# Kernel tuning notes

Measured on AMD Instinct MI355X. Metric: run time of the kernel, lower is better.

Reference implementation:

```python
import jax, jax.numpy as jnp
import numpy as np

B, C, IMG, P = 32, 3, 224, 16
D, DEPTH, N, K, E = 384, 12, 16, 4, 2
DI = E * D           # 768
R = (D + 15) // 16   # dt_rank = 24
L = (IMG // P) ** 2  # 196
NC = 1000


def _layernorm(x, g, b, eps=1e-5):
    mu = jnp.mean(x, axis=-1, keepdims=True)
    var = jnp.var(x, axis=-1, keepdims=True)
    return (x - mu) * jax.lax.rsqrt(var + eps) * g + b


def _block(x, p):
    bn_g, bn_b, in_w, conv_w, conv_b, xp_w, dtp_w, dtp_b, A_log, Dsk, out_w = p
    h = _layernorm(x, bn_g, bn_b)
    xz = h @ in_w                       # (B,L,2*DI)
    xc, z = xz[..., :DI], xz[..., DI:]
    # causal depthwise conv1d along L
    xpad = jnp.pad(xc, ((0, 0), (K - 1, 0), (0, 0)))
    xc = sum(conv_w[:, k] * xpad[:, k:k + L, :] for k in range(K)) + conv_b
    xc = jax.nn.silu(xc)
    dbc = xc @ xp_w                      # (B,L,R+2N)
    dt, Bm, Cm = dbc[..., :R], dbc[..., R:R + N], dbc[..., R + N:]
    dt = jax.nn.softplus(dt @ dtp_w + dtp_b)        # (B,L,DI)
    A = -jnp.exp(A_log)                              # (DI,N)
    da = jnp.exp(dt[..., None] * A)                  # (B,L,DI,N)
    db = dt[..., None] * Bm[:, :, None, :] * xc[..., None]
    def combine(c1, c2):
        a1, b1 = c1
        a2, b2 = c2
        return a1 * a2, a2 * b1 + b2
    _, hs = jax.lax.associative_scan(combine, (da, db), axis=1)
    y = jnp.einsum('blmn,bln->blm', hs, Cm) + Dsk * xc
    y = y * jax.nn.silu(z)
    return x + y @ out_w


def setup_inputs() -> dict:
    key = jax.random.key(0)
    ks = jax.random.split(key, 16)
    s = 0.02
    inp = {
        'x': jax.random.normal(ks[0], (B, C, IMG, IMG), jnp.float32),
        'patch_w': jax.random.normal(ks[1], (D, C, P, P), jnp.float32) * s,
        'patch_b': jnp.zeros((D,), jnp.float32),
        'pos_embed': jax.random.normal(ks[2], (1, L, D), jnp.float32) * s,
        'bn_g': jnp.ones((DEPTH, D), jnp.float32),
        'bn_b': jnp.zeros((DEPTH, D), jnp.float32),
        'in_w': jax.random.normal(ks[3], (DEPTH, D, 2 * DI), jnp.float32) * s,
        'conv_w': jax.random.normal(ks[4], (DEPTH, DI, K), jnp.float32) * s,
        'conv_b': jnp.zeros((DEPTH, DI), jnp.float32),
        'xp_w': jax.random.normal(ks[5], (DEPTH, DI, R + 2 * N), jnp.float32) * s,
        'dtp_w': jax.random.normal(ks[6], (DEPTH, R, DI), jnp.float32) * (R ** -0.5),
        'dtp_b': jax.random.uniform(ks[7], (DEPTH, DI), jnp.float32, -4.0, -1.0),
        'A_log': jnp.log(jnp.broadcast_to(jnp.arange(1, N + 1, dtype=jnp.float32), (DEPTH, DI, N))),
        'D_skip': jnp.ones((DEPTH, DI), jnp.float32),
        'out_w': jax.random.normal(ks[8], (DEPTH, DI, D), jnp.float32) * s,
        'norm_g': jnp.ones((D,), jnp.float32),
        'norm_b': jnp.zeros((D,), jnp.float32),
        'head_w': jax.random.normal(ks[9], (D, NC), jnp.float32) * s,
        'head_b': jnp.zeros((NC,), jnp.float32),
    }
    return inp


def reference(x, patch_w, patch_b, pos_embed, bn_g, bn_b, in_w, conv_w, conv_b,
              xp_w, dtp_w, dtp_b, A_log, D_skip, out_w, norm_g, norm_b, head_w, head_b):
    # patch embed: conv2d stride=patch -> (B,D,H',W') -> (B,L,D) + pos
    h = jax.lax.conv_general_dilated(x, patch_w, (P, P), 'VALID',
                                     dimension_numbers=('NCHW', 'OIHW', 'NCHW'))
    h = h + patch_b[None, :, None, None]
    h = h.reshape(B, D, L).transpose(0, 2, 1) + pos_embed
    params = (bn_g, bn_b, in_w, conv_w, conv_b, xp_w, dtp_w, dtp_b, A_log, D_skip, out_w)
    h, _ = jax.lax.scan(lambda c, p: (_block(c, p), None), h, params)
    h = _layernorm(h, norm_g, norm_b)
    feat = h.mean(axis=1)
    return feat @ head_w + head_b
```

## Files before the change

### kernel.cpp

```cpp
#include <hip/hip_runtime.h>
#include <math.h>

typedef short bf16x8 __attribute__((ext_vector_type(8)));
typedef float f32x4 __attribute__((ext_vector_type(4)));
typedef float f32x2 __attribute__((ext_vector_type(2)));
typedef unsigned short u16;
typedef unsigned int u32;
typedef unsigned short u16x4 __attribute__((ext_vector_type(4)));

#define B_    32
#define D_    384
#define DEPTH 12
#define NST   16
#define DI_   768
#define R_    24
#define L_    196
#define NC_   1000
#define M_    (B_*L_)
#define SEG   28
#define NSEG  7

__device__ __forceinline__ u16 f2bf(float f) {
  union { float f; unsigned u; } v; v.f = f;
  unsigned r = v.u + 0x7fffu + ((v.u >> 16) & 1u);
  return (u16)(r >> 16);
}
__device__ __forceinline__ float bf2f(u16 x) {
  union { unsigned u; float f; } v; v.u = ((unsigned)x) << 16;
  return v.f;
}
__device__ __forceinline__ float quad_sum(float y) {
  y += __int_as_float(__builtin_amdgcn_update_dpp(0, __float_as_int(y), 0xB1, 0xf, 0xf, true));
  y += __int_as_float(__builtin_amdgcn_update_dpp(0, __float_as_int(y), 0x4E, 0xf, 0xf, true));
  return y;
}

__global__ void k_transpose_bf16(const float* __restrict__ in, u16* __restrict__ out,
                                 int R, int C) {
  __shared__ float tile[32][33];
  const size_t zoff = (size_t)blockIdx.z * R * C;
  in  += zoff; out += zoff;
  int c0 = blockIdx.x * 32, r0 = blockIdx.y * 32;
  int tx = threadIdx.x, ty = threadIdx.y;
  for (int i = ty; i < 32; i += 8) {
    int r = r0 + i, c = c0 + tx;
    tile[i][tx] = (r < R && c < C) ? in[(size_t)r * C + c] : 0.f;
  }
  __syncthreads();
  for (int i = ty; i < 32; i += 8) {
    int c = c0 + i, r = r0 + tx;
    if (c < C && r < R) out[(size_t)c * R + r] = f2bf(tile[tx][i]);
  }
}

__global__ void k_convert_bf16(const float* __restrict__ in, u16* __restrict__ out, int n) {
  int i = blockIdx.x * 256 + threadIdx.x;
  if (i < n) out[i] = f2bf(in[i]);
}

__global__ void k_prepA(const float* __restrict__ alog, float* __restrict__ A, int n) {
  int i = blockIdx.x * 256 + threadIdx.x;
  if (i < n) A[i] = -__expf(alog[i]);
}

__global__ void k_im2col(const float* __restrict__ x, u16* __restrict__ xcol) {
  int idx = blockIdx.x * 256 + threadIdx.x;
  if (idx >= M_ * 768) return;
  int k = idx % 768, m = idx / 768;
  int b = m / L_, l = m % L_;
  int li = l / 14, lj = l % 14;
  int c = k / 256, r = k % 256;
  int i = r / 16, j = r % 16;
  int hh = li * 16 + i, ww = lj * 16 + j;
  xcol[idx] = f2bf(x[(((size_t)b * 3 + c) * 224 + hh) * 224 + ww]);
}

template<int BM, int BN, int EPI, int OB>
__global__ __launch_bounds__(256)
void k_gemm(const u16* __restrict__ A, const u16* __restrict__ BT,
            float* __restrict__ Cout, int Nn, int Kk,
            const float* __restrict__ bias, const float* __restrict__ pos) {
  const int m0 = blockIdx.x * BM;
  const int n0 = blockIdx.y * BN;
  __shared__ u16 lA[BM * 72];
  __shared__ u16 lB[BN * 72];
  const int tid  = threadIdx.x;
  const int wave = tid >> 6, lane = tid & 63;
  const int wm = (wave >> 1) * (BM / 2), wn = (wave & 1) * (BN / 2);
  constexpr int MI = BM / 32, NJ = BN / 32;
  constexpr int NV = (BM + BN) / 32;
  f32x4 acc[MI][NJ] = {};
  const int fr = lane & 15, kg = (lane >> 4) * 8;

  bf16x8 v[NV];
  auto load = [&](int k0) {
    #pragma unroll
    for (int q = 0; q < NV; ++q) {
      int id = tid + q * 256;
      int row = id >> 3, vv = id & 7;
      bf16x8 t = {};
      if (row < BM) {
        t = *(const bf16x8*)(A + (size_t)(m0 + row) * Kk + k0 + vv * 8);
      } else {
        int br = n0 + row - BM;
        if (br < Nn) t = *(const bf16x8*)(BT + (size_t)br * Kk + k0 + vv * 8);
      }
      v[q] = t;
    }
  };
  load(0);
  for (int k0 = 0; k0 < Kk; k0 += 64) {
    __syncthreads();
    #pragma unroll
    for (int q = 0; q < NV; ++q) {
      int id = tid + q * 256;
      int row = id >> 3, vv = id & 7;
      u16* dst = (row < BM) ? (lA + row * 72 + vv * 8) : (lB + (size_t)(row - BM) * 72 + vv * 8);
      *(bf16x8*)dst = v[q];
    }
    __syncthreads();
    if (k0 + 64 < Kk) load(k0 + 64);
    #pragma unroll
    for (int kk = 0; kk < 64; kk += 32) {
      bf16x8 af[MI], bfr[NJ];
      #pragma unroll
      for (int i = 0; i < MI; ++i)
        af[i] = *(const bf16x8*)(lA + (wm + i * 16 + fr) * 72 + kk + kg);
      #pragma unroll
      for (int j = 0; j < NJ; ++j)
        bfr[j] = *(const bf16x8*)(lB + (wn + j * 16 + fr) * 72 + kk + kg);
      #pragma unroll
      for (int i = 0; i < MI; ++i)
        #pragma unroll
        for (int j = 0; j < NJ; ++j)
          acc[i][j] = __builtin_amdgcn_mfma_f32_16x16x32_bf16(af[i], bfr[j], acc[i][j], 0, 0, 0);
    }
  }

  const int rg = (lane >> 4) * 4;
  #pragma unroll
  for (int i = 0; i < MI; ++i) {
    int row = m0 + wm + i * 16 + rg;
    #pragma unroll
    for (int j = 0; j < NJ; ++j) {
      int col = n0 + wn + j * 16 + fr;
      if (col >= Nn) continue;
      #pragma unroll
      for (int r = 0; r < 4; ++r) {
        float vv = acc[i][j][r];
        size_t idx = (size_t)(row + r) * Nn + col;
        if (EPI == 0) {
          if (OB) ((u16*)Cout)[idx] = f2bf(vv);
          else    Cout[idx] = vv;
        }
        else if (EPI == 1) Cout[idx] += vv;
        else               Cout[idx] = vv + bias[col] + pos[(size_t)((row + r) % L_) * Nn + col];
      }
    }
  }
}

__global__ __launch_bounds__(256)
void k_xp_split(const u16* __restrict__ A, const u16* __restrict__ BT,
                float* __restrict__ pbuf) {
  const int m0 = blockIdx.x * 32;
  const int ks = blockIdx.y;
  __shared__ u16 lA[32 * 72];
  __shared__ u16 lB[64 * 72];
  const int tid  = threadIdx.x;
  const int wave = tid >> 6, lane = tid & 63;
  const int wm = (wave >> 1) * 16, wn = (wave & 1) * 32;
  const int fr = lane & 15, kg = (lane >> 4) * 8;
  f32x4 acc[2] = {};

  bf16x8 v[3];
  auto load = [&](int k0) {
    #pragma unroll
    for (int q = 0; q < 3; ++q) {
      int id = tid + q * 256;
      int row = id >> 3, vv = id & 7;
      bf16x8 t = {};
      if (row < 32) {
        t = *(const bf16x8*)(A + (size_t)(m0 + row) * DI_ + k0 + vv * 8);
      } else {
        int br = row - 32;
        if (br < 56) t = *(const bf16x8*)(BT + (size_t)br * DI_ + k0 + vv * 8);
      }
      v[q] = t;
    }
  };
  const int kbase = ks * 192;
  load(kbase);
  for (int k0 = kbase; k0 < kbase + 192; k0 += 64) {
    __syncthreads();
    #pragma unroll
    for (int q = 0; q < 3; ++q) {
      int id = tid + q * 256;
      int row = id >> 3, vv = id & 7;
      u16* dst = (row < 32) ? (lA + row * 72 + vv * 8) : (lB + (size_t)(row - 32) * 72 + vv * 8);
      *(bf16x8*)dst = v[q];
    }
    __syncthreads();
    if (k0 + 64 < kbase + 192) load(k0 + 64);
    #pragma unroll
    for (int kk = 0; kk < 64; kk += 32) {
      bf16x8 af = *(const bf16x8*)(lA + (wm + fr) * 72 + kk + kg);
      bf16x8 b0 = *(const bf16x8*)(lB + (wn + fr) * 72 + kk + kg);
      bf16x8 b1 = *(const bf16x8*)(lB + (wn + 16 + fr) * 72 + kk + kg);
      acc[0] = __builtin_amdgcn_mfma_f32_16x16x32_bf16(af, b0, acc[0], 0, 0, 0);
      acc[1] = __builtin_amdgcn_mfma_f32_16x16x32_bf16(af, b1, acc[1], 0, 0, 0);
    }
  }
  const int rg = (lane >> 4) * 4;
  #pragma unroll
  for (int j = 0; j < 2; ++j) {
    int col = wn + j * 16 + fr;
    if (col >= 56) continue;
    #pragma unroll
    for (int r = 0; r < 4; ++r) {
      int row = wm + rg + r;
      pbuf[((size_t)ks * M_ + m0 + row) * 56 + col] = acc[j][r];
    }
  }
}

__global__ __launch_bounds__(384)
void k_ln(const float* __restrict__ x, const float* __restrict__ g,
          const float* __restrict__ bt, u16* __restrict__ h) {
  const int m = blockIdx.x, d = threadIdx.x;
  __shared__ float red[12];
  float v = x[(size_t)m * D_ + d];
  float s = v, s2 = v * v;
  #pragma unroll
  for (int o = 32; o > 0; o >>= 1) { s += __shfl_xor(s, o); s2 += __shfl_xor(s2, o); }
  int wid = d >> 6;
  if ((d & 63) == 0) { red[wid] = s; red[6 + wid] = s2; }
  __syncthreads();
  float ts = 0.f, ts2 = 0.f;
  #pragma unroll
  for (int w = 0; w < 6; ++w) { ts += red[w]; ts2 += red[6 + w]; }
  float mu = ts / (float)D_;
  float var = ts2 / (float)D_ - mu * mu;
  float rs = rsqrtf(var + 1e-5f);
  h[(size_t)m * D_ + d] = f2bf((v - mu) * rs * g[d] + bt[d]);
}

__global__ __launch_bounds__(256)
void k_conv(const u16* __restrict__ xzb, const float* __restrict__ cw,
            const float* __restrict__ cb, u16* __restrict__ xcb) {
  int idx = blockIdx.x * 256 + threadIdx.x;
  if (idx >= M_ * (DI_ / 4)) return;
  int dq = idx % (DI_ / 4), m = idx / (DI_ / 4), l = m % L_;
  int di4 = dq * 4;
  const u16* base = xzb + (size_t)m * 1536 + di4;
  float xv[4][4];
  #pragma unroll
  for (int t = 0; t < 4; ++t) {
    int back = 3 - t;
    u16x4 v = {};
    if (l >= back) v = *(const u16x4*)(base - (size_t)back * 1536);
    #pragma unroll
    for (int c = 0; c < 4; ++c) xv[t][c] = bf2f(v[c]);
  }
  f32x4 bv = *(const f32x4*)(cb + di4);
  u16x4 outv;
  #pragma unroll
  for (int c = 0; c < 4; ++c) {
    f32x4 w = *(const f32x4*)(cw + (size_t)(di4 + c) * 4);
    float acc = bv[c] + w[0] * xv[0][c] + w[1] * xv[1][c] + w[2] * xv[2][c] + w[3] * xv[3][c];
    float s = acc / (1.f + __expf(-acc));
    outv[c] = f2bf(s);
  }
  *(u16x4*)(xcb + (size_t)m * DI_ + di4) = outv;
}

__global__ __launch_bounds__(256)
void k_scan_part(const float* __restrict__ pbuf, const u16* __restrict__ xcb,
                 const float* __restrict__ dtw, const float* __restrict__ dtb,
                 const float* __restrict__ Abuf, const float* __restrict__ Dsk,
                 float* __restrict__ ys, float* __restrict__ hend,
                 float* __restrict__ send) {
  const int b   = blockIdx.x;
  const int di0 = blockIdx.y * 64;
  const int s   = blockIdx.z;
  const int tid = threadIdx.x;
  const int dil = tid >> 2, nq = tid & 3;
  const int di  = di0 + dil;
  __shared__ float sDT[SEG][64];
  __shared__ float sXC[SEG][64];
  __shared__ float sBC[SEG][32];
  __shared__ float sdb[SEG][28];

  const f32x4 Arow = *(const f32x4*)(Abuf + (size_t)di * NST + nq * 4);
  const float Dv = Dsk[di];
  const size_t mb = (size_t)b * L_ + (size_t)s * SEG;
  const int chd = tid & 63;

  {
    int r = tid >> 4, cc = (tid & 15) * 4;
    #pragma unroll
    for (int j = 0; j < 2; ++j) {
      int row = r + j * 16;
      if (row < SEG) {
        u16x4 xv = *(const u16x4*)(xcb + (mb + row) * DI_ + di0 + cc);
        f32x4 xf;
        #pragma unroll
        for (int q = 0; q < 4; ++q) xf[q] = bf2f(xv[q]);
        *(f32x4*)&sXC[row][cc] = xf;
      }
    }
    if (tid < SEG * 6) {
      int row = tid / 6, c4 = (tid % 6) * 4;
      f32x4 ssum = {};
      #pragma unroll
      for (int ks = 0; ks < 4; ++ks)
        ssum += *(const f32x4*)(pbuf + ((size_t)ks * M_ + mb + row) * 56 + c4);
      *(f32x4*)&sdb[row][c4] = ssum;
    }
    if (tid < SEG * 8) {
      int row = tid >> 3, c4 = (tid & 7) * 4;
      f32x4 ssum = {};
      #pragma unroll
      for (int ks = 0; ks < 4; ++ks)
        ssum += *(const f32x4*)(pbuf + ((size_t)ks * M_ + mb + row) * 56 + 24 + c4);
      *(f32x4*)&sBC[row][c4] = ssum;
    }
  }
  float w[24];
  #pragma unroll
  for (int r = 0; r < 24; ++r) w[r] = dtw[r * DI_ + di0 + chd];
  const float bvd = dtb[di0 + chd];
  __syncthreads();

  {
    const int rg = tid >> 6;
    #pragma unroll
    for (int rr = 0; rr < 7; ++rr) {
      int row = rg * 7 + rr;
      float acc = bvd;
      #pragma unroll
      for (int r4 = 0; r4 < 6; ++r4) {
        f32x4 sv = *(const f32x4*)&sdb[row][r4 * 4];
        acc += sv[0] * w[r4 * 4] + sv[1] * w[r4 * 4 + 1]
             + sv[2] * w[r4 * 4 + 2] + sv[3] * w[r4 * 4 + 3];
      }
      float e  = __expf(-fabsf(acc));
      sDT[row][chd] = fmaxf(acc, 0.f) + __logf(1.f + e);
    }
  }
  __syncthreads();

  float h[4] = {0.f, 0.f, 0.f, 0.f};
  float scum = 0.f;
  float dtc = sDT[0][dil], xcc = sXC[0][dil];
  f32x4 Bv = *(const f32x4*)&sBC[0][nq * 4];
  f32x4 Cv = *(const f32x4*)&sBC[0][16 + nq * 4];
  #pragma unroll 4
  for (int t = 0; t < SEG; ++t) {
    float dtn = 0.f, xcn = 0.f; f32x4 Bn = {}, Cn = {};
    if (t + 1 < SEG) {
      dtn = sDT[t + 1][dil]; xcn = sXC[t + 1][dil];
      Bn = *(const f32x4*)&sBC[t + 1][nq * 4];
      Cn = *(const f32x4*)&sBC[t + 1][16 + nq * 4];
    }
    scum += dtc;
    float dxv = dtc * xcc;
    float y = (nq == 0) ? Dv * xcc : 0.f;
    #pragma unroll
    for (int n = 0; n < 4; ++n) {
      float e = __expf(dtc * Arow[n]);
      h[n] = e * h[n] + dxv * Bv[n];
      y += h[n] * Cv[n];
    }
    y = quad_sum(y);
    if (nq == 0)
      *(f32x2*)(ys + (mb + t) * (DI_ * 2) + (size_t)(di0 + dil) * 2) = f32x2{y, scum};
    dtc = dtn; xcc = xcn; Bv = Bn; Cv = Cn;
  }

  size_t sb = ((size_t)s * B_ + b) * DI_ + di;
  *(f32x4*)(hend + sb * 16 + nq * 4) = f32x4{h[0], h[1], h[2], h[3]};
  if (nq == 0) send[sb] = scum;
}

__global__ __launch_bounds__(256)
void k_scan_apply(const float* __restrict__ pbuf, const float* __restrict__ ys,
                  const u16* __restrict__ xzb, const float* __restrict__ Abuf,
                  const float* __restrict__ hend, const float* __restrict__ send,
                  u16* __restrict__ yb) {
  const int b   = blockIdx.x;
  const int di0 = blockIdx.y * 64;
  const int s   = blockIdx.z;
  const int tid = threadIdx.x;
  const size_t mb = (size_t)b * L_ + (size_t)s * SEG;
  __shared__ float sC[SEG][16];
  __shared__ float sYO[SEG][64];

  if (s > 0) {
    const int dil = tid >> 2, nq = tid & 3;
    const f32x4 A4 = *(const f32x4*)(Abuf + (size_t)(di0 + dil) * NST + nq * 4);
    f32x4 H4 = {0.f, 0.f, 0.f, 0.f};
    for (int r = 0; r < s; ++r) {
      size_t sb = ((size_t)r * B_ + b) * DI_ + di0 + dil;
      f32x4 he = *(const f32x4*)(hend + sb * 16 + nq * 4);
      float se = send[sb];
      #pragma unroll
      for (int q = 0; q < 4; ++q) H4[q] = __expf(A4[q] * se) * H4[q] + he[q];
    }
    if (tid < SEG * 4) {
      int row = tid >> 2, qq = tid & 3;
      f32x4 ssum = {};
      #pragma unroll
      for (int ks = 0; ks < 4; ++ks)
        ssum += *(const f32x4*)(pbuf + ((size_t)ks * M_ + mb + row) * 56 + 40 + qq * 4);
      *(f32x4*)&sC[row][qq * 4] = ssum;
    }
    __syncthreads();
    #pragma unroll 4
    for (int l = 0; l < SEG; ++l) {
      f32x2 yp = *(const f32x2*)(ys + (mb + l) * (DI_ * 2) + (size_t)(di0 + dil) * 2);
      f32x4 C4 = *(const f32x4*)&sC[l][nq * 4];
      float scum = yp.y;
      float corr = 0.f;
      #pragma unroll
      for (int n = 0; n < 4; ++n) corr += C4[n] * __expf(A4[n] * scum) * H4[n];
      corr = quad_sum(corr);
      if (nq == 0) sYO[l][dil] = yp.x + corr;
    }
  } else {
    #pragma unroll
    for (int j = 0; j < 7; ++j) {
      int id = tid + j * 256;
      int row = id >> 6, ch = id & 63;
      sYO[row][ch] = ys[(mb + row) * (DI_ * 2) + (size_t)(di0 + ch) * 2];
    }
  }
  __syncthreads();
  #pragma unroll
  for (int j = 0; j < 4; ++j) {
    int id = tid + j * 256;
    if (id < SEG * 32) {
      int row = id >> 5, c2 = id & 31;
      int ch0 = c2 * 2;
      float y0 = sYO[row][ch0], y1 = sYO[row][ch0 + 1];
      u32 zz = *(const u32*)(xzb + (mb + row) * 1536 + DI_ + di0 + ch0);
      float z0 = bf2f((u16)(zz & 0xffff)), z1 = bf2f((u16)(zz >> 16));
      u32 o = (u32)f2bf(y0 * z0 / (1.f + __expf(-z0)))
            | ((u32)f2bf(y1 * z1 / (1.f + __expf(-z1))) << 16);
      *((u32*)yb + ((mb + row) * DI_ + di0) / 2 + c2) = o;
    }
  }
}

__global__ __launch_bounds__(384)
void k_feat_part(const float* __restrict__ x, float* __restrict__ partial) {
  const int b = blockIdx.x, j = blockIdx.y, d = threadIdx.x;
  __shared__ float red[12];
  const int l0 = j * 28;
  float acc = 0.f;
  float v = x[((size_t)b * L_ + l0) * D_ + d];
  for (int l = l0; l < l0 + 28; ++l) {
    float vn = (l + 1 < l0 + 28) ? x[((size_t)b * L_ + l + 1) * D_ + d] : 0.f;
    float s = v, s2 = v * v;
    #pragma unroll
    for (int o = 32; o > 0; o >>= 1) { s += __shfl_xor(s, o); s2 += __shfl_xor(s2, o); }
    int wid = d >> 6;
    if ((d & 63) == 0) { red[wid] = s; red[6 + wid] = s2; }
    __syncthreads();
    float ts = 0.f, ts2 = 0.f;
    #pragma unroll
    for (int w = 0; w < 6; ++w) { ts += red[w]; ts2 += red[6 + w]; }
    float mu = ts * (1.f / (float)D_);
    float var = ts2 * (1.f / (float)D_) - mu * mu;
    acc += (v - mu) * rsqrtf(var + 1e-5f);
    __syncthreads();
    v = vn;
  }
  partial[((size_t)(b * 7 + j)) * D_ + d] = acc;
}

__global__ __launch_bounds__(256)
void k_head(const float* __restrict__ partial, const float* __restrict__ g,
            const float* __restrict__ bt, const float* __restrict__ hw,
            const float* __restrict__ hb, float* __restrict__ out) {
  const int b = blockIdx.y;
  const int c = blockIdx.x * 256 + threadIdx.x;
  __shared__ float sf[D_];
  for (int i = threadIdx.x; i < D_; i += 256) {
    float s = 0.f;
    #pragma unroll
    for (int j = 0; j < 7; ++j) s += partial[((size_t)(b * 7 + j)) * D_ + i];
    sf[i] = g[i] * (s * (1.f / (float)L_)) + bt[i];
  }
  __syncthreads();
  if (c >= NC_) return;
  float acc = hb[c];
  for (int d = 0; d < D_; ++d) acc += sf[d] * hw[(size_t)d * NC_ + c];
  out[(size_t)b * NC_ + c] = acc;
}

extern "C" void kernel_launch(void* const* d_in, const int* in_sizes, int n_in,
                              void* d_out, int out_size, void* d_ws, size_t ws_size,
                              hipStream_t stream) {
  const float* x_in    = (const float*)d_in[0];
  const float* patch_w = (const float*)d_in[1];
  const float* patch_b = (const float*)d_in[2];
  const float* pos     = (const float*)d_in[3];
  const float* bn_g    = (const float*)d_in[4];
  const float* bn_b    = (const float*)d_in[5];
  const float* in_w    = (const float*)d_in[6];
  const float* conv_w  = (const float*)d_in[7];
  const float* conv_b  = (const float*)d_in[8];
  const float* xp_w    = (const float*)d_in[9];
  const float* dtp_w   = (const float*)d_in[10];
  const float* dtp_b   = (const float*)d_in[11];
  const float* A_log   = (const float*)d_in[12];
  const float* D_skip  = (const float*)d_in[13];
  const float* out_w   = (const float*)d_in[14];
  const float* norm_g  = (const float*)d_in[15];
  const float* norm_b  = (const float*)d_in[16];
  const float* head_w  = (const float*)d_in[17];
  const float* head_b  = (const float*)d_in[18];
  float* out = (float*)d_out;

  char* ws = (char*)d_ws;
  size_t off = 0;
  auto alloc = [&](size_t bytes) { size_t o = off; off += (bytes + 255) & ~(size_t)255; return o; };

  float* xbuf   = (float*)(ws + alloc((size_t)M_ * D_ * 4));
  u16*   hbuf   = (u16*)  (ws + alloc((size_t)M_ * D_ * 2));
  u16*   xzb    = (u16*)  (ws + alloc((size_t)M_ * 1536 * 2));
  u16*   xcbb   = (u16*)  (ws + alloc((size_t)M_ * DI_ * 2));
  float* pbuf   = (float*)(ws + alloc((size_t)4 * M_ * 56 * 4));
  u16*   im2col = (u16*)  (ws + alloc((size_t)M_ * 768 * 2));
  u16*   ybuf   = (u16*)  (ws + alloc((size_t)M_ * DI_ * 2));
  float* ysbuf  = (float*)(ws + alloc((size_t)M_ * DI_ * 2 * 4));
  float* hend   = (float*)(ws + alloc((size_t)NSEG * B_ * DI_ * NST * 4));
  float* send   = (float*)(ws + alloc((size_t)NSEG * B_ * DI_ * 4));
  float* Abuf   = (float*)(ws + alloc((size_t)DEPTH * DI_ * NST * 4));
  float* partial= (float*)(ws + alloc((size_t)B_ * 7 * D_ * 4));
  u16*   in_wT  = (u16*)  (ws + alloc((size_t)DEPTH * 1536 * D_ * 2));
  u16*   xp_wT  = (u16*)  (ws + alloc((size_t)DEPTH * 56 * DI_ * 2));
  u16*   out_wT = (u16*)  (ws + alloc((size_t)DEPTH * D_ * DI_ * 2));
  u16*   pw_b   = (u16*)  (ws + alloc((size_t)D_ * 768 * 2));

  dim3 tb(32, 8);
  k_transpose_bf16<<<dim3(48, 12, DEPTH), tb, 0, stream>>>(in_w,  in_wT,  D_, 1536);
  k_transpose_bf16<<<dim3(2, 24, DEPTH),  tb, 0, stream>>>(xp_w,  xp_wT,  DI_, 56);
  k_transpose_bf16<<<dim3(12, 24, DEPTH), tb, 0, stream>>>(out_w, out_wT, DI_, D_);
  k_convert_bf16<<<(D_ * 768 + 255) / 256, 256, 0, stream>>>(patch_w, pw_b, D_ * 768);
  k_prepA<<<(DEPTH * DI_ * NST + 255) / 256, 256, 0, stream>>>(A_log, Abuf, DEPTH * DI_ * NST);

  k_im2col<<<(M_ * 768 + 255) / 256, 256, 0, stream>>>(x_in, im2col);
  k_gemm<64,64,2,0><<<dim3(M_ / 64, 6), 256, 0, stream>>>(im2col, pw_b, xbuf, D_, 768, patch_b, pos);

  for (int dp = 0; dp < DEPTH; ++dp) {
    const u16* iwt = in_wT  + (size_t)dp * 1536 * D_;
    const u16* xwt = xp_wT  + (size_t)dp * 56 * DI_;
    const u16* owt = out_wT + (size_t)dp * D_ * DI_;
    const float* Al = Abuf + (size_t)dp * DI_ * NST;
    k_ln<<<M_, 384, 0, stream>>>(xbuf, bn_g + dp * D_, bn_b + dp * D_, hbuf);
    k_gemm<64,128,0,1><<<dim3(M_ / 64, 12), 256, 0, stream>>>(hbuf, iwt, (float*)xzb, 1536, D_, nullptr, nullptr);
    k_conv<<<(M_ * (DI_ / 4) + 255) / 256, 256, 0, stream>>>(xzb, conv_w + (size_t)dp * DI_ * 4,
                                                             conv_b + dp * DI_, xcbb);
    k_xp_split<<<dim3(M_ / 32, 4), 256, 0, stream>>>(xcbb, xwt, pbuf);
    k_scan_part<<<dim3(B_, DI_ / 64, NSEG), 256, 0, stream>>>(pbuf, xcbb,
                                                              dtp_w + (size_t)dp * R_ * DI_,
                                                              dtp_b + dp * DI_, Al,
                                                              D_skip + dp * DI_, ysbuf, hend, send);
    k_scan_apply<<<dim3(B_, DI_ / 64, NSEG), 256, 0, stream>>>(pbuf, ysbuf, xzb, Al,
                                                               hend, send, ybuf);
    k_gemm<64,64,1,0><<<dim3(M_ / 64, 6), 256, 0, stream>>>(ybuf, owt, xbuf, D_, DI_, nullptr, nullptr);
  }

  k_feat_part<<<dim3(B_, 7), 384, 0, stream>>>(xbuf, partial);
  k_head<<<dim3((NC_ + 255) / 256, B_), 256, 0, stream>>>(partial, norm_g, norm_b, head_w, head_b, out);
}
```

Baseline: 1.471 ms.

## Restructure chunked scan into state pass then full recompute pass

The two-pass segmented scan now runs a lightweight first kernel that computes only each segment's end state and cumulative dt. The second kernel folds in the prefix states and reruns the full scan with the correct initial state, writing gated outputs directly. This removes the large fp32 intermediate buffer of per-step outputs and cumulative dt, and the correction exponentials in the apply pass. In exchange the dt projection and the input loads are recomputed in both kernels.

```diff
diff --git a/kernel.cpp b/kernel.cpp
--- a/kernel.cpp
+++ b/kernel.cpp
@@ -275,11 +275,111 @@
 }
 
 __global__ __launch_bounds__(256)
-void k_scan_part(const float* __restrict__ pbuf, const u16* __restrict__ xcb,
-                 const float* __restrict__ dtw, const float* __restrict__ dtb,
-                 const float* __restrict__ Abuf, const float* __restrict__ Dsk,
-                 float* __restrict__ ys, float* __restrict__ hend,
-                 float* __restrict__ send) {
+void k_scan_state(const float* __restrict__ pbuf, const u16* __restrict__ xcb,
+                  const float* __restrict__ dtw, const float* __restrict__ dtb,
+                  const float* __restrict__ Abuf, float* __restrict__ hend,
+                  float* __restrict__ send) {
+  const int b   = blockIdx.x;
+  const int di0 = blockIdx.y * 64;
+  const int s   = blockIdx.z;
+  const int tid = threadIdx.x;
+  const int dil = tid >> 2, nq = tid & 3;
+  const int di  = di0 + dil;
+  __shared__ float sDT[SEG][64];
+  __shared__ float sXC[SEG][64];
+  __shared__ float sB [SEG][16];
+  __shared__ float sdb[SEG][28];
+
+  const f32x4 Arow = *(const f32x4*)(Abuf + (size_t)di * NST + nq * 4);
+  const size_t mb = (size_t)b * L_ + (size_t)s * SEG;
+  const int chd = tid & 63;
+
+  {
+    int r = tid >> 4, cc = (tid & 15) * 4;
+    #pragma unroll
+    for (int j = 0; j < 2; ++j) {
+      int row = r + j * 16;
+      if (row < SEG) {
+        u16x4 xv = *(const u16x4*)(xcb + (mb + row) * DI_ + di0 + cc);
+        f32x4 xf;
+        #pragma unroll
+        for (int q = 0; q < 4; ++q) xf[q] = bf2f(xv[q]);
+        *(f32x4*)&sXC[row][cc] = xf;
+      }
+    }
+    if (tid < SEG * 6) {
+      int row = tid / 6, c4 = (tid % 6) * 4;
+      f32x4 ssum = {};
+      #pragma unroll
+      for (int ks = 0; ks < 4; ++ks)
+        ssum += *(const f32x4*)(pbuf + ((size_t)ks * M_ + mb + row) * 56 + c4);
+      *(f32x4*)&sdb[row][c4] = ssum;
+    }
+    if (tid < SEG * 4) {
+      int row = tid >> 2, c4 = (tid & 3) * 4;
+      f32x4 ssum = {};
+      #pragma unroll
+      for (int ks = 0; ks < 4; ++ks)
+        ssum += *(const f32x4*)(pbuf + ((size_t)ks * M_ + mb + row) * 56 + 24 + c4);
+      *(f32x4*)&sB[row][c4] = ssum;
+    }
+  }
+  float w[24];
+  #pragma unroll
+  for (int r = 0; r < 24; ++r) w[r] = dtw[r * DI_ + di0 + chd];
+  const float bvd = dtb[di0 + chd];
+  __syncthreads();
+
+  {
+    const int rg = tid >> 6;
+    #pragma unroll
+    for (int rr = 0; rr < 7; ++rr) {
+      int row = rg * 7 + rr;
+      float acc = bvd;
+      #pragma unroll
+      for (int r4 = 0; r4 < 6; ++r4) {
+        f32x4 sv = *(const f32x4*)&sdb[row][r4 * 4];
+        acc += sv[0] * w[r4 * 4] + sv[1] * w[r4 * 4 + 1]
+             + sv[2] * w[r4 * 4 + 2] + sv[3] * w[r4 * 4 + 3];
+      }
+      float e  = __expf(-fabsf(acc));
+      sDT[row][chd] = fmaxf(acc, 0.f) + __logf(1.f + e);
+    }
+  }
+  __syncthreads();
+
+  float h[4] = {0.f, 0.f, 0.f, 0.f};
+  float scum = 0.f;
+  float dtc = sDT[0][dil], xcc = sXC[0][dil];
+  f32x4 Bv = *(const f32x4*)&sB[0][nq * 4];
+  #pragma unroll 4
+  for (int t = 0; t < SEG; ++t) {
+    float dtn = 0.f, xcn = 0.f; f32x4 Bn = {};
+    if (t + 1 < SEG) {
+      dtn = sDT[t + 1][dil]; xcn = sXC[t + 1][dil];
+      Bn = *(const f32x4*)&sB[t + 1][nq * 4];
+    }
+    scum += dtc;
+    float dxv = dtc * xcc;
+    #pragma unroll
+    for (int n = 0; n < 4; ++n) {
+      float e = __expf(dtc * Arow[n]);
+      h[n] = e * h[n] + dxv * Bv[n];
+    }
+    dtc = dtn; xcc = xcn; Bv = Bn;
+  }
+
+  size_t sb = ((size_t)s * B_ + b) * DI_ + di;
+  *(f32x4*)(hend + sb * 16 + nq * 4) = f32x4{h[0], h[1], h[2], h[3]};
+  if (nq == 0) send[sb] = scum;
+}
+
+__global__ __launch_bounds__(256)
+void k_scan_full(const float* __restrict__ pbuf, const u16* __restrict__ xcb,
+                 const u16* __restrict__ xzb, const float* __restrict__ dtw,
+                 const float* __restrict__ dtb, const float* __restrict__ Abuf,
+                 const float* __restrict__ Dsk, const float* __restrict__ hend,
+                 const float* __restrict__ send, u16* __restrict__ yb) {
   const int b   = blockIdx.x;
   const int di0 = blockIdx.y * 64;
   const int s   = blockIdx.z;
@@ -290,6 +390,7 @@
   __shared__ float sXC[SEG][64];
   __shared__ float sBC[SEG][32];
   __shared__ float sdb[SEG][28];
+  __shared__ float sYO[SEG][64];
 
   const f32x4 Arow = *(const f32x4*)(Abuf + (size_t)di * NST + nq * 4);
   const float Dv = Dsk[di];
@@ -326,6 +427,16 @@
       *(f32x4*)&sBC[row][c4] = ssum;
     }
   }
+
+  float h[4] = {0.f, 0.f, 0.f, 0.f};
+  for (int r = 0; r < s; ++r) {
+    size_t sb = ((size_t)r * B_ + b) * DI_ + di;
+    f32x4 he = *(const f32x4*)(hend + sb * 16 + nq * 4);
+    float se = send[sb];
+    #pragma unroll
+    for (int q = 0; q < 4; ++q) h[q] = __expf(Arow[q] * se) * h[q] + he[q];
+  }
+
   float w[24];
   #pragma unroll
   for (int r = 0; r < 24; ++r) w[r] = dtw[r * DI_ + di0 + chd];
@@ -350,8 +461,6 @@
   }
   __syncthreads();
 
-  float h[4] = {0.f, 0.f, 0.f, 0.f};
-  float scum = 0.f;
   float dtc = sDT[0][dil], xcc = sXC[0][dil];
   f32x4 Bv = *(const f32x4*)&sBC[0][nq * 4];
   f32x4 Cv = *(const f32x4*)&sBC[0][16 + nq * 4];
@@ -363,7 +472,6 @@
       Bn = *(const f32x4*)&sBC[t + 1][nq * 4];
       Cn = *(const f32x4*)&sBC[t + 1][16 + nq * 4];
     }
-    scum += dtc;
     float dxv = dtc * xcc;
     float y = (nq == 0) ? Dv * xcc : 0.f;
     #pragma unroll
@@ -373,69 +481,11 @@
       y += h[n] * Cv[n];
     }
     y = quad_sum(y);
-    if (nq == 0)
-      *(f32x2*)(ys + (mb + t) * (DI_ * 2) + (size_t)(di0 + dil) * 2) = f32x2{y, scum};
+    if (nq == 0) sYO[t][dil] = y;
     dtc = dtn; xcc = xcn; Bv = Bn; Cv = Cn;
   }
-
-  size_t sb = ((size_t)s * B_ + b) * DI_ + di;
-  *(f32x4*)(hend + sb * 16 + nq * 4) = f32x4{h[0], h[1], h[2], h[3]};
-  if (nq == 0) send[sb] = scum;
-}
-
-__global__ __launch_bounds__(256)
-void k_scan_apply(const float* __restrict__ pbuf, const float* __restrict__ ys,
-                  const u16* __restrict__ xzb, const float* __restrict__ Abuf,
-                  const float* __restrict__ hend, const float* __restrict__ send,
-                  u16* __restrict__ yb) {
-  const int b   = blockIdx.x;
-  const int di0 = blockIdx.y * 64;
-  const int s   = blockIdx.z;
-  const int tid = threadIdx.x;
-  const size_t mb = (size_t)b * L_ + (size_t)s * SEG;
-  __shared__ float sC[SEG][16];
-  __shared__ float sYO[SEG][64];
-
-  if (s > 0) {
-    const int dil = tid >> 2, nq = tid & 3;
-    const f32x4 A4 = *(const f32x4*)(Abuf + (size_t)(di0 + dil) * NST + nq * 4);
-    f32x4 H4 = {0.f, 0.f, 0.f, 0.f};
-    for (int r = 0; r < s; ++r) {
-      size_t sb = ((size_t)r * B_ + b) * DI_ + di0 + dil;
-      f32x4 he = *(const f32x4*)(hend + sb * 16 + nq * 4);
-      float se = send[sb];
-      #pragma unroll
-      for (int q = 0; q < 4; ++q) H4[q] = __expf(A4[q] * se) * H4[q] + he[q];
-    }
-    if (tid < SEG * 4) {
-      int row = tid >> 2, qq = tid & 3;
-      f32x4 ssum = {};
-      #pragma unroll
-      for (int ks = 0; ks < 4; ++ks)
-        ssum += *(const f32x4*)(pbuf + ((size_t)ks * M_ + mb + row) * 56 + 40 + qq * 4);
-      *(f32x4*)&sC[row][qq * 4] = ssum;
-    }
-    __syncthreads();
-    #pragma unroll 4
-    for (int l = 0; l < SEG; ++l) {
-      f32x2 yp = *(const f32x2*)(ys + (mb + l) * (DI_ * 2) + (size_t)(di0 + dil) * 2);
-      f32x4 C4 = *(const f32x4*)&sC[l][nq * 4];
-      float scum = yp.y;
-      float corr = 0.f;
-      #pragma unroll
-      for (int n = 0; n < 4; ++n) corr += C4[n] * __expf(A4[n] * scum) * H4[n];
-      corr = quad_sum(corr);
-      if (nq == 0) sYO[l][dil] = yp.x + corr;
-    }
-  } else {
-    #pragma unroll
-    for (int j = 0; j < 7; ++j) {
-      int id = tid + j * 256;
-      int row = id >> 6, ch = id & 63;
-      sYO[row][ch] = ys[(mb + row) * (DI_ * 2) + (size_t)(di0 + ch) * 2];
-    }
-  }
-  __syncthreads();
+  __syncthreads();
+
   #pragma unroll
   for (int j = 0; j < 4; ++j) {
     int id = tid + j * 256;
@@ -534,7 +584,6 @@
   float* pbuf   = (float*)(ws + alloc((size_t)4 * M_ * 56 * 4));
   u16*   im2col = (u16*)  (ws + alloc((size_t)M_ * 768 * 2));
   u16*   ybuf   = (u16*)  (ws + alloc((size_t)M_ * DI_ * 2));
-  float* ysbuf  = (float*)(ws + alloc((size_t)M_ * DI_ * 2 * 4));
   float* hend   = (float*)(ws + alloc((size_t)NSEG * B_ * DI_ * NST * 4));
   float* send   = (float*)(ws + alloc((size_t)NSEG * B_ * DI_ * 4));
   float* Abuf   = (float*)(ws + alloc((size_t)DEPTH * DI_ * NST * 4));
@@ -559,17 +608,17 @@
     const u16* xwt = xp_wT  + (size_t)dp * 56 * DI_;
     const u16* owt = out_wT + (size_t)dp * D_ * DI_;
     const float* Al = Abuf + (size_t)dp * DI_ * NST;
+    const float* dw = dtp_w + (size_t)dp * R_ * DI_;
+    const float* db = dtp_b + dp * DI_;
     k_ln<<<M_, 384, 0, stream>>>(xbuf, bn_g + dp * D_, bn_b + dp * D_, hbuf);
     k_gemm<64,128,0,1><<<dim3(M_ / 64, 12), 256, 0, stream>>>(hbuf, iwt, (float*)xzb, 1536, D_, nullptr, nullptr);
     k_conv<<<(M_ * (DI_ / 4) + 255) / 256, 256, 0, stream>>>(xzb, conv_w + (size_t)dp * DI_ * 4,
                                                              conv_b + dp * DI_, xcbb);
     k_xp_split<<<dim3(M_ / 32, 4), 256, 0, stream>>>(xcbb, xwt, pbuf);
-    k_scan_part<<<dim3(B_, DI_ / 64, NSEG), 256, 0, stream>>>(pbuf, xcbb,
-                                                              dtp_w + (size_t)dp * R_ * DI_,
-                                                              dtp_b + dp * DI_, Al,
-                                                              D_skip + dp * DI_, ysbuf, hend, send);
-    k_scan_apply<<<dim3(B_, DI_ / 64, NSEG), 256, 0, stream>>>(pbuf, ysbuf, xzb, Al,
-                                                               hend, send, ybuf);
+    k_scan_state<<<dim3(B_, DI_ / 64, NSEG - 1), 256, 0, stream>>>(pbuf, xcbb, dw, db, Al,
+                                                                   hend, send);
+    k_scan_full<<<dim3(B_, DI_ / 64, NSEG), 256, 0, stream>>>(pbuf, xcbb, xzb, dw, db, Al,
+                                                              D_skip + dp * DI_, hend, send, ybuf);
     k_gemm<64,64,1,0><<<dim3(M_ / 64, 6), 256, 0, stream>>>(ybuf, owt, xbuf, D_, DI_, nullptr, nullptr);
   }
 
```

Result: faster. 1.371 ms (-6.8%).
